# Performance work log

Hardware: AMD Instinct MI355X
Metric: run time of the kernel (lower is better)

Reference implementation:

```python
import jax, jax.numpy as jnp
import numpy as np

# ---- config (matches init_kwargs) ----
DIM = 1024
HEADS = 8            # local_heads == heads
QK_HD = 128          # qk_head_dim
V_HD = 128           # v_head_dim
NOPE = 64            # qk_nope_head_dim
ROPE = 64            # qk_rope_head_dim
KV_LORA = 256
N_EXP = 32
N_GROUPS = 8
TOPK = 4             # n_activated_experts
TOPK_GROUPS = 4
INTER = 512
N_SHARED = 1
ROUTE_SCALE = 1.0
EPS = 1e-6


def rmsnorm(x, w):
    xf = x.astype(jnp.float32)
    rms = jnp.sqrt(jnp.mean(xf ** 2, axis=-1, keepdims=True) + EPS)
    return (xf / rms * w).astype(x.dtype)


def setup_inputs() -> dict:
    key = jax.random.key(0)
    ks = jax.random.split(key, 16)
    s = 0.02
    return {
        "x": jax.random.normal(ks[0], (2, 1024, DIM), jnp.float32),
        # attention sub-layer params
        "norm_attn": jnp.ones((DIM,), jnp.float32),
        "wq": jax.random.normal(ks[1], (DIM, HEADS * QK_HD), jnp.float32) * s,
        "wkv_a": jax.random.normal(ks[2], (DIM, KV_LORA + ROPE), jnp.float32) * s,
        "kv_norm_w": jnp.ones((KV_LORA,), jnp.float32),
        "wkv_b": jax.random.normal(ks[3], (KV_LORA, HEADS * (NOPE + V_HD)), jnp.float32) * s,
        "wo": jax.random.normal(ks[4], (HEADS * V_HD, DIM), jnp.float32) * s,
        # MoE sub-layer params
        "norm_moe": jnp.ones((DIM,), jnp.float32),
        "gate_w": jax.random.normal(ks[5], (N_EXP, DIM), jnp.float32) * 0.01,
        "gate_b": jnp.zeros((N_EXP,), jnp.float32),
        "ew1": jax.random.normal(ks[6], (N_EXP, DIM, INTER), jnp.float32) * s,
        "ew2": jax.random.normal(ks[7], (N_EXP, INTER, DIM), jnp.float32) * s,
        "ew3": jax.random.normal(ks[8], (N_EXP, DIM, INTER), jnp.float32) * s,
        "sw1": jax.random.normal(ks[9], (DIM, N_SHARED * INTER), jnp.float32) * s,
        "sw2": jax.random.normal(ks[10], (N_SHARED * INTER, DIM), jnp.float32) * s,
        "sw3": jax.random.normal(ks[11], (DIM, N_SHARED * INTER), jnp.float32) * s,
    }


def _mla(x, wq, wkv_a, kv_norm_w, wkv_b, wo):
    B, S, _ = x.shape
    # q_lora_rank == 0 -> direct q projection; nope/rope split+concat is identity
    q = (x @ wq).reshape(B, S, HEADS, QK_HD)
    kv = x @ wkv_a                                   # [B,S,KV_LORA+ROPE]
    c, k_pe = kv[..., :KV_LORA], kv[..., KV_LORA:]
    kvp = (rmsnorm(c, kv_norm_w) @ wkv_b).reshape(B, S, HEADS, NOPE + V_HD)
    k_nope, v = kvp[..., :NOPE], kvp[..., NOPE:]
    k = jnp.concatenate(
        [k_nope, jnp.broadcast_to(k_pe[:, :, None, :], (B, S, HEADS, ROPE))], axis=-1)
    out = jax.nn.dot_product_attention(q, k, v, scale=QK_HD ** -0.5, is_causal=True)
    return out.reshape(B, S, -1) @ wo


def _gate(xf, gate_w, gate_b):
    T = xf.shape[0]
    scores = jax.nn.sigmoid(xf @ gate_w.T)           # [T,E]
    original = scores
    s = scores + gate_b
    # hierarchical group selection: top-2 score sum per group, keep top groups
    sg = s.reshape(T, N_GROUPS, -1)
    group_score = jnp.sort(sg, axis=-1)[..., -2:].sum(axis=-1)
    group_idx = jnp.argsort(group_score, axis=-1)[..., -TOPK_GROUPS:]
    mask = jnp.ones((T, N_GROUPS), bool).at[jnp.arange(T)[:, None], group_idx].set(False)
    s = jnp.where(mask[..., None], -jnp.inf, sg).reshape(T, -1)
    indices = jnp.argsort(s, axis=-1)[..., -TOPK:]   # [T,K]
    w = jnp.take_along_axis(original, indices, axis=1)
    w = w / (w.sum(axis=-1, keepdims=True) + 1e-20)  # sigmoid normalization
    return w * ROUTE_SCALE, indices


def _moe(xf, gate_w, gate_b, ew1, ew2, ew3, sw1, sw2, sw3):
    # dense all-expert SwiGLU as in the original (nn.vmap over axis_size=E)
    weights, indices = _gate(xf, gate_w, gate_b)
    h = jax.nn.silu(jnp.einsum('td,edh->eth', xf, ew1)) * jnp.einsum('td,edh->eth', xf, ew3)
    all_out = jnp.einsum('eth,ehd->etd', h, ew2)     # [E,T,dim]
    # per-token gather of its top-k experts, weighted combine
    selected = jnp.take_along_axis(all_out.transpose(1, 0, 2), indices[:, :, None], axis=1)  # [T,K,dim]
    y = (selected * weights[..., None]).sum(axis=1)
    z = (jax.nn.silu(xf @ sw1) * (xf @ sw3)) @ sw2   # shared expert MLP
    return y + z


def reference(x, norm_attn, wq, wkv_a, kv_norm_w, wkv_b, wo,
              norm_moe, gate_w, gate_b, ew1, ew2, ew3, sw1, sw2, sw3):
    # MLA layer: x + MLA(RMSNorm(x))
    x = x + _mla(rmsnorm(x, norm_attn), wq, wkv_a, kv_norm_w, wkv_b, wo)
    # MoE layer: x + MoE(RMSNorm(x))
    shape = x.shape
    xf = rmsnorm(x, norm_moe).reshape(-1, DIM)
    y = _moe(xf, gate_w, gate_b, ew1, ew2, ew3, sw1, sw2, sw3)
    return x + y.reshape(shape)
```

## Files before the change

kernel.cpp:

```cpp
#include <hip/hip_runtime.h>
#include <hip/hip_bf16.h>

#define T_TOK 2048
#define DIM 1024
#define HEADS 8
#define QK_HD 128
#define V_HD 128
#define NOPE 64
#define ROPE 64
#define KV_LORA 256
#define N_EXP 32
#define TOPK 4
#define INTER 512
#define S_LEN 1024
#define KVP_W (HEADS * (NOPE + V_HD))

typedef __attribute__((ext_vector_type(8))) _Float16 f16x8;
typedef __attribute__((ext_vector_type(4))) float f32x4;

__device__ inline unsigned short f2h(float f) {
  union { _Float16 h; unsigned short u; } c;
  c.h = (_Float16)f;
  return c.u;
}
__device__ inline float h2f(unsigned short u) {
  union { _Float16 h; unsigned short u; } c;
  c.u = u;
  return (float)c.h;
}

__device__ inline int swz(int row, int col) {
  return row * 64 + (col ^ (((row & 7) ^ ((row & 3) << 1)) << 3));
}

__launch_bounds__(256)
__global__ void tcvt_k(const float* __restrict__ src, unsigned short* __restrict__ dst,
                       int K, int N) {
  int e = blockIdx.z;
  src += (size_t)e * K * N;
  dst += (size_t)e * K * N;
  int n0 = blockIdx.x * 32, k0 = blockIdx.y * 32;
  __shared__ float ts[32][33];
  int tid = threadIdx.x;
  int r = tid >> 3, c4 = (tid & 7) * 4;
  float4 v = *(const float4*)(src + (size_t)(k0 + r) * N + n0 + c4);
  ts[r][c4] = v.x; ts[r][c4 + 1] = v.y; ts[r][c4 + 2] = v.z; ts[r][c4 + 3] = v.w;
  __syncthreads();
  ushort4 o;
  o.x = f2h(ts[c4][r]);
  o.y = f2h(ts[c4 + 1][r]);
  o.z = f2h(ts[c4 + 2][r]);
  o.w = f2h(ts[c4 + 3][r]);
  *(ushort4*)(dst + (size_t)(n0 + r) * K + k0 + c4) = o;
}

__launch_bounds__(64)
__global__ void zero_counters_k(int* __restrict__ counts, int* __restrict__ fill) {
  int i = threadIdx.x;
  if (i < N_EXP) { counts[i] = 0; fill[i] = 0; }
}

__launch_bounds__(256)
__global__ void rmsnorm_k(const float* __restrict__ x, int in_stride, int width,
                          const float* __restrict__ w, unsigned short* __restrict__ out,
                          float* __restrict__ out2, int out_stride) {
  int row = blockIdx.x;
  const float* xr = x + (size_t)row * in_stride;
  float ss = 0.f;
  for (int i = threadIdx.x; i < width; i += 256) { float v = xr[i]; ss += v * v; }
  #pragma unroll
  for (int off = 32; off; off >>= 1) ss += __shfl_down(ss, off, 64);
  __shared__ float red[4];
  if ((threadIdx.x & 63) == 0) red[threadIdx.x >> 6] = ss;
  __syncthreads();
  if (threadIdx.x == 0) {
    float tot = red[0] + red[1] + red[2] + red[3];
    red[0] = rsqrtf(tot / (float)width + 1e-6f);
  }
  __syncthreads();
  float scale = red[0];
  for (int i = threadIdx.x; i < width; i += 256) {
    float v = xr[i] * scale * w[i];
    out[(size_t)row * out_stride + i] = f2h(v);
    if (out2) out2[(size_t)row * out_stride + i] = v;
  }
}

template <int RES, int OUTH>
__launch_bounds__(256)
__global__ void gemm_bt_k(const unsigned short* __restrict__ A,
                          const unsigned short* __restrict__ B,
                          const float* __restrict__ R, void* __restrict__ Cout,
                          int N, int K) {
  const int n0 = blockIdx.x * 64;
  const int m0 = blockIdx.y * 64;
  __shared__ __align__(16) unsigned short As[64 * 64];
  __shared__ __align__(16) unsigned short Bs[64 * 64];
  const int tid = threadIdx.x;
  const int lane = tid & 63, wave = tid >> 6;
  const int quad = lane >> 4, lm = lane & 15;
  const int wm = (wave >> 1) * 32, wn = (wave & 1) * 32;
  f32x4 acc[2][2] = {};
  const int sr = tid >> 2, sc = tid & 3;
  const unsigned short* Ap = A + (size_t)(m0 + sr) * K;
  const unsigned short* Bp = B + (size_t)(n0 + sr) * K;
  f16x8 a0 = *(const f16x8*)(Ap + sc * 8);
  f16x8 a1 = *(const f16x8*)(Ap + sc * 8 + 32);
  f16x8 b0 = *(const f16x8*)(Bp + sc * 8);
  f16x8 b1 = *(const f16x8*)(Bp + sc * 8 + 32);
  for (int k0 = 0; k0 < K; k0 += 64) {
    __syncthreads();
    *(f16x8*)&As[swz(sr, sc * 8)] = a0;
    *(f16x8*)&As[swz(sr, sc * 8 + 32)] = a1;
    *(f16x8*)&Bs[swz(sr, sc * 8)] = b0;
    *(f16x8*)&Bs[swz(sr, sc * 8 + 32)] = b1;
    __syncthreads();
    const int kn = k0 + 64;
    if (kn < K) {
      a0 = *(const f16x8*)(Ap + kn + sc * 8);
      a1 = *(const f16x8*)(Ap + kn + sc * 8 + 32);
      b0 = *(const f16x8*)(Bp + kn + sc * 8);
      b1 = *(const f16x8*)(Bp + kn + sc * 8 + 32);
    }
    #pragma unroll
    for (int ks = 0; ks < 2; ks++) {
      f16x8 af0 = *(const f16x8*)&As[swz(wm + lm, ks * 32 + quad * 8)];
      f16x8 af1 = *(const f16x8*)&As[swz(wm + 16 + lm, ks * 32 + quad * 8)];
      f16x8 bf0 = *(const f16x8*)&Bs[swz(wn + lm, ks * 32 + quad * 8)];
      f16x8 bf1 = *(const f16x8*)&Bs[swz(wn + 16 + lm, ks * 32 + quad * 8)];
      acc[0][0] = __builtin_amdgcn_mfma_f32_16x16x32_f16(af0, bf0, acc[0][0], 0, 0, 0);
      acc[0][1] = __builtin_amdgcn_mfma_f32_16x16x32_f16(af0, bf1, acc[0][1], 0, 0, 0);
      acc[1][0] = __builtin_amdgcn_mfma_f32_16x16x32_f16(af1, bf0, acc[1][0], 0, 0, 0);
      acc[1][1] = __builtin_amdgcn_mfma_f32_16x16x32_f16(af1, bf1, acc[1][1], 0, 0, 0);
    }
  }
  #pragma unroll
  for (int i = 0; i < 2; i++)
    #pragma unroll
    for (int j = 0; j < 2; j++) {
      int row = m0 + wm + i * 16 + quad * 4;
      int col = n0 + wn + j * 16 + lm;
      #pragma unroll
      for (int r = 0; r < 4; r++) {
        float v = acc[i][j][r];
        if (RES) v += R[(size_t)(row + r) * N + col];
        if (OUTH) ((unsigned short*)Cout)[(size_t)(row + r) * N + col] = f2h(v);
        else ((float*)Cout)[(size_t)(row + r) * N + col] = v;
      }
    }
}

__launch_bounds__(256)
__global__ void moe_up_k(const unsigned short* __restrict__ xfb,
                         const unsigned short* __restrict__ w1t,
                         const unsigned short* __restrict__ w3t,
                         unsigned short* __restrict__ hout,
                         const int* __restrict__ perm, const int* __restrict__ offs,
                         int Mfull) {
  const int e = blockIdx.z;
  int base = 0, count = Mfull;
  if (offs) { base = offs[e]; count = offs[e + 1] - base; }
  const int m0 = blockIdx.y * 64;
  if (m0 >= count) return;
  const int n0 = blockIdx.x * 64;
  const unsigned short* W1 = w1t + (size_t)e * (INTER * DIM);
  const unsigned short* W3 = w3t + (size_t)e * (INTER * DIM);
  __shared__ __align__(16) unsigned short As[64 * 64];
  __shared__ __align__(16) unsigned short B1s[64 * 64];
  __shared__ __align__(16) unsigned short B2s[64 * 64];
  __shared__ int toks[64];
  const int tid = threadIdx.x;
  if (tid < 64) {
    int g = m0 + tid;
    toks[tid] = (g < count) ? (perm ? (perm[base + g] >> 2) : g) : -1;
  }
  __syncthreads();
  const int lane = tid & 63, wave = tid >> 6;
  const int quad = lane >> 4, lm = lane & 15;
  const int wm = (wave >> 1) * 32, wn = (wave & 1) * 32;
  f32x4 acc1[2][2] = {};
  f32x4 acc2[2][2] = {};
  const int sr = tid >> 2, sc = tid & 3;
  const int tok = toks[sr];
  const unsigned short* Ap = xfb + (size_t)(tok < 0 ? 0 : tok) * DIM;
  const bool av = (tok >= 0);
  const unsigned short* B1p = W1 + (size_t)(n0 + sr) * DIM;
  const unsigned short* B2p = W3 + (size_t)(n0 + sr) * DIM;
  f16x8 a0 = {0,0,0,0,0,0,0,0}, a1 = {0,0,0,0,0,0,0,0};
  if (av) {
    a0 = *(const f16x8*)(Ap + sc * 8);
    a1 = *(const f16x8*)(Ap + sc * 8 + 32);
  }
  f16x8 b10 = *(const f16x8*)(B1p + sc * 8);
  f16x8 b11 = *(const f16x8*)(B1p + sc * 8 + 32);
  f16x8 b20 = *(const f16x8*)(B2p + sc * 8);
  f16x8 b21 = *(const f16x8*)(B2p + sc * 8 + 32);
  for (int k0 = 0; k0 < DIM; k0 += 64) {
    __syncthreads();
    *(f16x8*)&As[swz(sr, sc * 8)] = a0;
    *(f16x8*)&As[swz(sr, sc * 8 + 32)] = a1;
    *(f16x8*)&B1s[swz(sr, sc * 8)] = b10;
    *(f16x8*)&B1s[swz(sr, sc * 8 + 32)] = b11;
    *(f16x8*)&B2s[swz(sr, sc * 8)] = b20;
    *(f16x8*)&B2s[swz(sr, sc * 8 + 32)] = b21;
    __syncthreads();
    const int kn = k0 + 64;
    if (kn < DIM) {
      if (av) {
        a0 = *(const f16x8*)(Ap + kn + sc * 8);
        a1 = *(const f16x8*)(Ap + kn + sc * 8 + 32);
      }
      b10 = *(const f16x8*)(B1p + kn + sc * 8);
      b11 = *(const f16x8*)(B1p + kn + sc * 8 + 32);
      b20 = *(const f16x8*)(B2p + kn + sc * 8);
      b21 = *(const f16x8*)(B2p + kn + sc * 8 + 32);
    }
    #pragma unroll
    for (int ks = 0; ks < 2; ks++) {
      f16x8 af0 = *(const f16x8*)&As[swz(wm + lm, ks * 32 + quad * 8)];
      f16x8 af1 = *(const f16x8*)&As[swz(wm + 16 + lm, ks * 32 + quad * 8)];
      f16x8 b1f0 = *(const f16x8*)&B1s[swz(wn + lm, ks * 32 + quad * 8)];
      f16x8 b1f1 = *(const f16x8*)&B1s[swz(wn + 16 + lm, ks * 32 + quad * 8)];
      f16x8 b2f0 = *(const f16x8*)&B2s[swz(wn + lm, ks * 32 + quad * 8)];
      f16x8 b2f1 = *(const f16x8*)&B2s[swz(wn + 16 + lm, ks * 32 + quad * 8)];
      acc1[0][0] = __builtin_amdgcn_mfma_f32_16x16x32_f16(af0, b1f0, acc1[0][0], 0, 0, 0);
      acc1[0][1] = __builtin_amdgcn_mfma_f32_16x16x32_f16(af0, b1f1, acc1[0][1], 0, 0, 0);
      acc1[1][0] = __builtin_amdgcn_mfma_f32_16x16x32_f16(af1, b1f0, acc1[1][0], 0, 0, 0);
      acc1[1][1] = __builtin_amdgcn_mfma_f32_16x16x32_f16(af1, b1f1, acc1[1][1], 0, 0, 0);
      acc2[0][0] = __builtin_amdgcn_mfma_f32_16x16x32_f16(af0, b2f0, acc2[0][0], 0, 0, 0);
      acc2[0][1] = __builtin_amdgcn_mfma_f32_16x16x32_f16(af0, b2f1, acc2[0][1], 0, 0, 0);
      acc2[1][0] = __builtin_amdgcn_mfma_f32_16x16x32_f16(af1, b2f0, acc2[1][0], 0, 0, 0);
      acc2[1][1] = __builtin_amdgcn_mfma_f32_16x16x32_f16(af1, b2f1, acc2[1][1], 0, 0, 0);
    }
  }
  #pragma unroll
  for (int i = 0; i < 2; i++)
    #pragma unroll
    for (int j = 0; j < 2; j++) {
      int col = n0 + wn + j * 16 + lm;
      #pragma unroll
      for (int r = 0; r < 4; r++) {
        int g = m0 + wm + i * 16 + quad * 4 + r;
        if (g < count) {
          float u = acc1[i][j][r];
          float vv = acc2[i][j][r];
          float h = (u / (1.f + __expf(-u))) * vv;
          hout[(size_t)(base + g) * INTER + col] = f2h(h);
        }
      }
    }
}

__launch_bounds__(256)
__global__ void moe_down_k(const unsigned short* __restrict__ hbuf,
                           const unsigned short* __restrict__ w2t,
                           unsigned short* __restrict__ dout,
                           const int* __restrict__ offs, int Mfull) {
  const int e = blockIdx.z;
  int base = 0, count = Mfull;
  if (offs) { base = offs[e]; count = offs[e + 1] - base; }
  const int m0 = blockIdx.y * 64;
  if (m0 >= count) return;
  const int n0 = blockIdx.x * 64;
  const unsigned short* W2 = w2t + (size_t)e * (DIM * INTER);
  __shared__ __align__(16) unsigned short As[64 * 64];
  __shared__ __align__(16) unsigned short Bs[64 * 64];
  const int tid = threadIdx.x;
  const int lane = tid & 63, wave = tid >> 6;
  const int quad = lane >> 4, lm = lane & 15;
  const int wm = (wave >> 1) * 32, wn = (wave & 1) * 32;
  f32x4 acc[2][2] = {};
  const int sr = tid >> 2, sc = tid & 3;
  const int g_s = m0 + sr;
  const bool av = (g_s < count);
  const unsigned short* Ap = hbuf + (size_t)(base + (av ? g_s : 0)) * INTER;
  const unsigned short* Bp = W2 + (size_t)(n0 + sr) * INTER;
  f16x8 a0 = {0,0,0,0,0,0,0,0}, a1 = {0,0,0,0,0,0,0,0};
  if (av) {
    a0 = *(const f16x8*)(Ap + sc * 8);
    a1 = *(const f16x8*)(Ap + sc * 8 + 32);
  }
  f16x8 b0 = *(const f16x8*)(Bp + sc * 8);
  f16x8 b1 = *(const f16x8*)(Bp + sc * 8 + 32);
  for (int k0 = 0; k0 < INTER; k0 += 64) {
    __syncthreads();
    *(f16x8*)&As[swz(sr, sc * 8)] = a0;
    *(f16x8*)&As[swz(sr, sc * 8 + 32)] = a1;
    *(f16x8*)&Bs[swz(sr, sc * 8)] = b0;
    *(f16x8*)&Bs[swz(sr, sc * 8 + 32)] = b1;
    __syncthreads();
    const int kn = k0 + 64;
    if (kn < INTER) {
      if (av) {
        a0 = *(const f16x8*)(Ap + kn + sc * 8);
        a1 = *(const f16x8*)(Ap + kn + sc * 8 + 32);
      }
      b0 = *(const f16x8*)(Bp + kn + sc * 8);
      b1 = *(const f16x8*)(Bp + kn + sc * 8 + 32);
    }
    #pragma unroll
    for (int ks = 0; ks < 2; ks++) {
      f16x8 af0 = *(const f16x8*)&As[swz(wm + lm, ks * 32 + quad * 8)];
      f16x8 af1 = *(const f16x8*)&As[swz(wm + 16 + lm, ks * 32 + quad * 8)];
      f16x8 bf0 = *(const f16x8*)&Bs[swz(wn + lm, ks * 32 + quad * 8)];
      f16x8 bf1 = *(const f16x8*)&Bs[swz(wn + 16 + lm, ks * 32 + quad * 8)];
      acc[0][0] = __builtin_amdgcn_mfma_f32_16x16x32_f16(af0, bf0, acc[0][0], 0, 0, 0);
      acc[0][1] = __builtin_amdgcn_mfma_f32_16x16x32_f16(af0, bf1, acc[0][1], 0, 0, 0);
      acc[1][0] = __builtin_amdgcn_mfma_f32_16x16x32_f16(af1, bf0, acc[1][0], 0, 0, 0);
      acc[1][1] = __builtin_amdgcn_mfma_f32_16x16x32_f16(af1, bf1, acc[1][1], 0, 0, 0);
    }
  }
  #pragma unroll
  for (int i = 0; i < 2; i++)
    #pragma unroll
    for (int j = 0; j < 2; j++) {
      int col = n0 + wn + j * 16 + lm;
      #pragma unroll
      for (int r = 0; r < 4; r++) {
        int g = m0 + wm + i * 16 + quad * 4 + r;
        if (g < count)
          dout[(size_t)(base + g) * DIM + col] = f2h(acc[i][j][r]);
      }
    }
}

__launch_bounds__(256)
__global__ void vtrans_k(const unsigned short* __restrict__ kvp,
                         unsigned short* __restrict__ vT) {
  const int z = blockIdx.z, h = z & 7, b = z >> 3;
  const int s0 = blockIdx.x * 32, d0 = blockIdx.y * 32;
  __shared__ unsigned short ts[32][36];
  const int tid = threadIdx.x;
  const int r = tid >> 3, c4 = (tid & 7) * 4;
  ushort4 v = *(const ushort4*)(kvp + (size_t)(b * S_LEN + s0 + r) * KVP_W + h * 192 + 64 + d0 + c4);
  ts[r][c4] = v.x; ts[r][c4 + 1] = v.y; ts[r][c4 + 2] = v.z; ts[r][c4 + 3] = v.w;
  __syncthreads();
  ushort4 o;
  o.x = ts[c4][r]; o.y = ts[c4 + 1][r]; o.z = ts[c4 + 2][r]; o.w = ts[c4 + 3][r];
  *(ushort4*)(vT + ((size_t)z * 128 + d0 + r) * S_LEN + s0 + c4) = o;
}

__launch_bounds__(256)
__global__ void attn_part_k(const unsigned short* __restrict__ q,
                            const unsigned short* __restrict__ kvp,
                            const float* __restrict__ kvb,
                            const unsigned short* __restrict__ vT,
                            float* __restrict__ opart, float* __restrict__ ml) {
  const int qt = blockIdx.x, ch = blockIdx.y, z = blockIdx.z;
  const int kt0 = ch * 4;
  if (kt0 > qt) return;
  const int h = z & 7, b = z >> 3;
  __shared__ __align__(16) _Float16 Ks[64][136];
  __shared__ __align__(16) _Float16 Vt[128][72];
  __shared__ __align__(16) _Float16 Ps[4][16][72];
  const int tid = threadIdx.x;
  const int lane = tid & 63, wave = tid >> 6;
  const int quad = lane >> 4, lm = lane & 15;
  const int qr0 = wave * 16;
  const float scale = 0.08838834764831845f;
  const int tq = b * S_LEN + qt * 64;

  f16x8 qf[4];
  #pragma unroll
  for (int kc = 0; kc < 4; kc++)
    qf[kc] = *(const f16x8*)(q + (size_t)(tq + qr0 + lm) * 1024 + h * 128 + kc * 32 + quad * 8);

  float m_i[4], l_i[4];
  #pragma unroll
  for (int r = 0; r < 4; r++) { m_i[r] = -1e30f; l_i[r] = 0.f; }
  f32x4 o_acc[8] = {};

  const int kt_end = (kt0 + 3 < qt) ? (kt0 + 3) : qt;
  for (int kt = kt0; kt <= kt_end; ++kt) {
    const int tk = b * S_LEN + kt * 64;
    for (int i = tid; i < 64 * 8; i += 256) {
      int key = i & 63, g = i >> 6;
      *(f16x8*)&Ks[key][g * 8] =
          *(const f16x8*)(kvp + (size_t)(tk + key) * KVP_W + h * 192 + g * 8);
    }
    for (int i = tid; i < 64 * 16; i += 256) {
      int key = i & 63, g = i >> 6;
      float4 v = *(const float4*)(kvb + (size_t)(tk + key) * 320 + 256 + g * 4);
      ushort4 u;
      u.x = f2h(v.x); u.y = f2h(v.y); u.z = f2h(v.z); u.w = f2h(v.w);
      *(ushort4*)&Ks[key][64 + g * 4] = u;
    }
    for (int i = tid; i < 128 * 8; i += 256) {
      int d = i >> 3, seg = i & 7;
      *(f16x8*)&Vt[d][seg * 8] =
          *(const f16x8*)(vT + ((size_t)z * 128 + d) * S_LEN + kt * 64 + seg * 8);
    }
    __syncthreads();

    f32x4 sacc[4] = {};
    #pragma unroll
    for (int kc = 0; kc < 4; kc++) {
      #pragma unroll
      for (int jn = 0; jn < 4; jn++) {
        f16x8 bf = *(const f16x8*)&Ks[jn * 16 + lm][kc * 32 + quad * 8];
        sacc[jn] = __builtin_amdgcn_mfma_f32_16x16x32_f16(qf[kc], bf, sacc[jn], 0, 0, 0);
      }
    }
    const bool diag = (kt == qt);
    float p[4][4];
    float rowmax[4], rowsum[4];
    #pragma unroll
    for (int r = 0; r < 4; r++) rowmax[r] = -1e30f;
    #pragma unroll
    for (int jn = 0; jn < 4; jn++)
      #pragma unroll
      for (int r = 0; r < 4; r++) {
        float s = sacc[jn][r] * scale;
        if (diag && (jn * 16 + lm > qr0 + quad * 4 + r)) s = -1e30f;
        p[jn][r] = s;
        rowmax[r] = fmaxf(rowmax[r], s);
      }
    #pragma unroll
    for (int m = 1; m < 16; m <<= 1)
      #pragma unroll
      for (int r = 0; r < 4; r++)
        rowmax[r] = fmaxf(rowmax[r], __shfl_xor(rowmax[r], m, 64));
    float al[4];
    #pragma unroll
    for (int r = 0; r < 4; r++) {
      float mn = fmaxf(m_i[r], rowmax[r]);
      al[r] = __expf(m_i[r] - mn);
      m_i[r] = mn;
      rowsum[r] = 0.f;
    }
    #pragma unroll
    for (int jn = 0; jn < 4; jn++)
      #pragma unroll
      for (int r = 0; r < 4; r++) {
        float pv = __expf(p[jn][r] - m_i[r]);
        p[jn][r] = pv;
        rowsum[r] += pv;
      }
    #pragma unroll
    for (int m = 1; m < 16; m <<= 1)
      #pragma unroll
      for (int r = 0; r < 4; r++)
        rowsum[r] += __shfl_xor(rowsum[r], m, 64);
    #pragma unroll
    for (int r = 0; r < 4; r++) l_i[r] = l_i[r] * al[r] + rowsum[r];
    #pragma unroll
    for (int jn2 = 0; jn2 < 8; jn2++)
      #pragma unroll
      for (int r = 0; r < 4; r++) o_acc[jn2][r] *= al[r];
    #pragma unroll
    for (int jn = 0; jn < 4; jn++)
      #pragma unroll
      for (int r = 0; r < 4; r++)
        Ps[wave][quad * 4 + r][jn * 16 + lm] = (_Float16)p[jn][r];
    #pragma unroll
    for (int kc = 0; kc < 2; kc++) {
      f16x8 af = *(const f16x8*)&Ps[wave][lm][kc * 32 + quad * 8];
      #pragma unroll
      for (int jn2 = 0; jn2 < 8; jn2++) {
        f16x8 bf = *(const f16x8*)&Vt[jn2 * 16 + lm][kc * 32 + quad * 8];
        o_acc[jn2] = __builtin_amdgcn_mfma_f32_16x16x32_f16(af, bf, o_acc[jn2], 0, 0, 0);
      }
    }
    __syncthreads();
  }

  const size_t slot = ((size_t)z * 16 + qt) * 4 + ch;
  float* op = opart + slot * 8192;
  #pragma unroll
  for (int jn2 = 0; jn2 < 8; jn2++) {
    int col = jn2 * 16 + lm;
    #pragma unroll
    for (int r = 0; r < 4; r++) {
      int row = qr0 + quad * 4 + r;
      op[(size_t)row * 128 + col] = o_acc[jn2][r];
    }
  }
  if (lm == 0) {
    #pragma unroll
    for (int r = 0; r < 4; r++) {
      int row = qr0 + quad * 4 + r;
      ml[slot * 128 + row * 2] = m_i[r];
      ml[slot * 128 + row * 2 + 1] = l_i[r];
    }
  }
}

__launch_bounds__(256)
__global__ void attn_comb_k(const float* __restrict__ opart, const float* __restrict__ ml,
                            unsigned short* __restrict__ o) {
  const int qt = blockIdx.x, z = blockIdx.y;
  const int h = z & 7, b = z >> 3;
  const int nch = (qt >> 2) + 1;
  const int tid = threadIdx.x;
  const int colg = tid & 31;
  const int tq = b * S_LEN + qt * 64;
  const size_t slotbase = ((size_t)z * 16 + qt) * 4;
  for (int row = tid >> 5; row < 64; row += 8) {
    float mmax = -1e30f;
    #pragma unroll
    for (int c = 0; c < 4; c++)
      if (c < nch) mmax = fmaxf(mmax, ml[(slotbase + c) * 128 + row * 2]);
    float w[4];
    float lsum = 0.f;
    #pragma unroll
    for (int c = 0; c < 4; c++) {
      if (c < nch) {
        float mc = ml[(slotbase + c) * 128 + row * 2];
        float lc = ml[(slotbase + c) * 128 + row * 2 + 1];
        w[c] = __expf(mc - mmax);
        lsum += lc * w[c];
      } else w[c] = 0.f;
    }
    float inv = 1.f / lsum;
    float ax = 0.f, ay = 0.f, az = 0.f, aw = 0.f;
    #pragma unroll
    for (int c = 0; c < 4; c++) {
      if (c < nch) {
        const float* op = opart + (slotbase + c) * 8192 + (size_t)row * 128 + colg * 4;
        float4 v = *(const float4*)op;
        ax += w[c] * v.x; ay += w[c] * v.y; az += w[c] * v.z; aw += w[c] * v.w;
      }
    }
    ushort4 u;
    u.x = f2h(ax * inv); u.y = f2h(ay * inv);
    u.z = f2h(az * inv); u.w = f2h(aw * inv);
    *(ushort4*)(o + (size_t)(tq + row) * 1024 + h * 128 + colg * 4) = u;
  }
}

__launch_bounds__(256)
__global__ void scores_k(const float* __restrict__ xf, const float* __restrict__ gw,
                         float* __restrict__ sc) {
  __shared__ float xls[32][129];
  __shared__ float gls[32][129];
  const int t0 = blockIdx.x * 32;
  const int tid = threadIdx.x;
  const int lr = tid >> 3, lc = tid & 7;
  const int e = tid & 31, tg = tid >> 5;
  float acc[4] = {};
  for (int k0 = 0; k0 < DIM; k0 += 128) {
    __syncthreads();
    #pragma unroll
    for (int it = 0; it < 4; it++) {
      int col = lc * 4 + it * 32;
      *(float4*)&xls[lr][col] = *(const float4*)(xf + (size_t)(t0 + lr) * DIM + k0 + col);
      *(float4*)&gls[lr][col] = *(const float4*)(gw + (size_t)lr * DIM + k0 + col);
    }
    __syncthreads();
    for (int d = 0; d < 128; d++) {
      float g = gls[e][d];
      #pragma unroll
      for (int j = 0; j < 4; j++)
        acc[j] += xls[tg * 4 + j][d] * g;
    }
  }
  #pragma unroll
  for (int j = 0; j < 4; j++)
    sc[(size_t)(t0 + tg * 4 + j) * N_EXP + e] = acc[j];
}

__launch_bounds__(64)
__global__ void route_k(const float* __restrict__ sc, const float* __restrict__ gb,
                        float* __restrict__ tw, int* __restrict__ tidx,
                        int* __restrict__ counts) {
  int t = blockIdx.x * 64 + threadIdx.x;
  if (t >= T_TOK) return;
  float orig[N_EXP], sb[N_EXP];
  #pragma unroll
  for (int i = 0; i < N_EXP; i++) {
    float s = 1.f / (1.f + __expf(-sc[(size_t)t * N_EXP + i]));
    orig[i] = s;
    sb[i] = s + gb[i];
  }
  float gsc[8];
  #pragma unroll
  for (int g = 0; g < 8; g++) {
    float m1 = -1e30f, m2 = -1e30f;
    #pragma unroll
    for (int j = 0; j < 4; j++) {
      float v = sb[g * 4 + j];
      if (v > m1) { m2 = m1; m1 = v; } else if (v > m2) m2 = v;
    }
    gsc[g] = m1 + m2;
  }
  unsigned gok = 0;
  #pragma unroll
  for (int it = 0; it < 4; it++) {
    int best = 0; float bv = -1e30f;
    #pragma unroll
    for (int g = 0; g < 8; g++)
      if (!((gok >> g) & 1u) && gsc[g] >= bv) { bv = gsc[g]; best = g; }
    gok |= 1u << best;
  }
  unsigned emask = 0;
  #pragma unroll
  for (int g = 0; g < 8; g++)
    if ((gok >> g) & 1u) emask |= 0xFu << (g * 4);
  unsigned taken = 0;
  int idx[TOPK]; float ow[TOPK]; float wsum = 0.f;
  #pragma unroll
  for (int k = 0; k < TOPK; k++) {
    int best = 0; float bv = -1e30f, bo = 0.f;
    #pragma unroll
    for (int i = 0; i < N_EXP; i++)
      if (((emask >> i) & 1u) && !((taken >> i) & 1u) && sb[i] >= bv) {
        bv = sb[i]; best = i; bo = orig[i];
      }
    taken |= 1u << best;
    idx[k] = best; ow[k] = bo; wsum += bo;
  }
  float inv = 1.f / (wsum + 1e-20f);
  #pragma unroll
  for (int k = 0; k < TOPK; k++) {
    tidx[t * TOPK + k] = idx[k];
    tw[t * TOPK + k] = ow[k] * inv;
    atomicAdd(&counts[idx[k]], 1);
  }
}

__global__ void scan_k(const int* __restrict__ counts, int* __restrict__ offs) {
  if (threadIdx.x == 0 && blockIdx.x == 0) {
    int acc = 0;
    for (int e = 0; e < N_EXP; e++) { offs[e] = acc; acc += counts[e]; }
    offs[N_EXP] = acc;
  }
}

__launch_bounds__(256)
__global__ void scatter_k(const int* __restrict__ tidx, const int* __restrict__ offs,
                          int* __restrict__ fill, int* __restrict__ perm,
                          int* __restrict__ posOf) {
  int t = blockIdx.x * 256 + threadIdx.x;
  if (t >= T_TOK) return;
  for (int j = 0; j < TOPK; j++) {
    int e = tidx[t * TOPK + j];
    int pos = atomicAdd(&fill[e], 1);
    int p = offs[e] + pos;
    perm[p] = t * TOPK + j;
    posOf[t * TOPK + j] = p;
  }
}

__launch_bounds__(256)
__global__ void final_gather_k(const float* __restrict__ x1,
                               const unsigned short* __restrict__ dbuf,
                               const unsigned short* __restrict__ sdbuf,
                               const int* __restrict__ posOf,
                               const float* __restrict__ tw,
                               float* __restrict__ out) {
  int t = blockIdx.x;
  int c0 = threadIdx.x * 4;
  int p0 = posOf[t * 4 + 0], p1 = posOf[t * 4 + 1];
  int p2 = posOf[t * 4 + 2], p3 = posOf[t * 4 + 3];
  float w0 = tw[t * 4 + 0], w1 = tw[t * 4 + 1];
  float w2 = tw[t * 4 + 2], w3 = tw[t * 4 + 3];
  size_t tb = (size_t)t * DIM;
  #pragma unroll
  for (int i = 0; i < 4; i++) {
    int c = c0 + i;
    float v = x1[tb + c] + h2f(sdbuf[tb + c])
            + w0 * h2f(dbuf[(size_t)p0 * DIM + c])
            + w1 * h2f(dbuf[(size_t)p1 * DIM + c])
            + w2 * h2f(dbuf[(size_t)p2 * DIM + c])
            + w3 * h2f(dbuf[(size_t)p3 * DIM + c]);
    out[tb + c] = v;
  }
}

extern "C" void kernel_launch(void* const* d_in, const int* in_sizes, int n_in,
                              void* d_out, int out_size, void* d_ws, size_t ws_size,
                              hipStream_t stream) {
  const float* x        = (const float*)d_in[0];
  const float* norm_attn= (const float*)d_in[1];
  const float* wq       = (const float*)d_in[2];
  const float* wkv_a    = (const float*)d_in[3];
  const float* kv_norm_w= (const float*)d_in[4];
  const float* wkv_b    = (const float*)d_in[5];
  const float* wo       = (const float*)d_in[6];
  const float* norm_moe = (const float*)d_in[7];
  const float* gate_w   = (const float*)d_in[8];
  const float* gate_b   = (const float*)d_in[9];
  const float* ew1      = (const float*)d_in[10];
  const float* ew2      = (const float*)d_in[11];
  const float* ew3      = (const float*)d_in[12];
  const float* sw1      = (const float*)d_in[13];
  const float* sw2      = (const float*)d_in[14];
  const float* sw3      = (const float*)d_in[15];
  float* out = (float*)d_out;

  char* wp = (char*)d_ws;
  auto alloc = [&](size_t bytes) -> char* {
    char* r = wp;
    wp += (bytes + 255) & ~(size_t)255;
    return r;
  };
  typedef unsigned short us;
  us* wqT   = (us*)alloc(1048576 * 2);
  us* wkvaT = (us*)alloc(327680 * 2);
  us* wkvbT = (us*)alloc(393216 * 2);
  us* woT   = (us*)alloc(1048576 * 2);
  us* ew1T  = (us*)alloc((size_t)16777216 * 2);
  us* ew3T  = (us*)alloc((size_t)16777216 * 2);
  us* ew2T  = (us*)alloc((size_t)16777216 * 2);
  us* sw1T  = (us*)alloc(524288 * 2);
  us* sw3T  = (us*)alloc(524288 * 2);
  us* sw2T  = (us*)alloc(524288 * 2);
  us* xb    = (us*)alloc(2097152 * 2);
  us* cn    = (us*)alloc(524288 * 2);
  us* atn   = (us*)alloc(2097152 * 2);
  us* dbuf  = (us*)alloc((size_t)8388608 * 2);
  us* qb    = (us*)alloc(2097152 * 4);
  float* kvb  = (float*)alloc(655360 * 4);
  us* kvp   = (us*)alloc(3145728 * 4);
  float* x1   = (float*)alloc(2097152 * 4);
  float* xf32 = (float*)alloc(2097152 * 4);
  float* scb  = (float*)alloc(65536 * 4);
  float* twb  = (float*)alloc(8192 * 4);
  int* tidx   = (int*)alloc(8192 * 4);
  int* perm   = (int*)alloc(8192 * 4);
  int* posOf  = (int*)alloc(8192 * 4);
  int* counts = (int*)alloc(64 * 4);
  int* offs   = (int*)alloc(64 * 4);
  int* fill   = (int*)alloc(64 * 4);
  us* vT     = (us*)alloc((size_t)2 * 8 * 128 * 1024 * 2);
  float* mlb = (float*)alloc((size_t)1024 * 128 * 4);
  us* sdbuf = qb;
  us* hbuf  = kvp;
  us* hs    = hbuf + (size_t)8192 * 512;
  float* opart = (float*)ew1T;

  tcvt_k<<<dim3(32, 32, 1), 256, 0, stream>>>(wq, wqT, 1024, 1024);
  tcvt_k<<<dim3(10, 32, 1), 256, 0, stream>>>(wkv_a, wkvaT, 1024, 320);
  tcvt_k<<<dim3(48, 8, 1), 256, 0, stream>>>(wkv_b, wkvbT, 256, 1536);
  tcvt_k<<<dim3(32, 32, 1), 256, 0, stream>>>(wo, woT, 1024, 1024);

  rmsnorm_k<<<T_TOK, 256, 0, stream>>>(x, DIM, DIM, norm_attn, xb, nullptr, DIM);
  gemm_bt_k<0, 1><<<dim3(16, 32), 256, 0, stream>>>(xb, wqT, nullptr, qb, 1024, 1024);
  gemm_bt_k<0, 0><<<dim3(5, 32), 256, 0, stream>>>(xb, wkvaT, nullptr, kvb, 320, 1024);
  rmsnorm_k<<<T_TOK, 256, 0, stream>>>(kvb, 320, KV_LORA, kv_norm_w, cn, nullptr, KV_LORA);
  gemm_bt_k<0, 1><<<dim3(24, 32), 256, 0, stream>>>(cn, wkvbT, nullptr, kvp, 1536, 256);
  vtrans_k<<<dim3(32, 4, 16), 256, 0, stream>>>(kvp, vT);
  attn_part_k<<<dim3(16, 4, 16), 256, 0, stream>>>(qb, kvp, kvb, vT, opart, mlb);
  attn_comb_k<<<dim3(16, 16), 256, 0, stream>>>(opart, mlb, atn);
  gemm_bt_k<1, 0><<<dim3(16, 32), 256, 0, stream>>>(atn, woT, x, x1, 1024, 1024);

  tcvt_k<<<dim3(16, 32, 32), 256, 0, stream>>>(ew1, ew1T, 1024, 512);
  tcvt_k<<<dim3(16, 32, 32), 256, 0, stream>>>(ew3, ew3T, 1024, 512);
  tcvt_k<<<dim3(32, 16, 32), 256, 0, stream>>>(ew2, ew2T, 512, 1024);
  tcvt_k<<<dim3(16, 32, 1), 256, 0, stream>>>(sw1, sw1T, 1024, 512);
  tcvt_k<<<dim3(16, 32, 1), 256, 0, stream>>>(sw3, sw3T, 1024, 512);
  tcvt_k<<<dim3(32, 16, 1), 256, 0, stream>>>(sw2, sw2T, 512, 1024);

  rmsnorm_k<<<T_TOK, 256, 0, stream>>>(x1, DIM, DIM, norm_moe, xb, xf32, DIM);
  zero_counters_k<<<1, 64, 0, stream>>>(counts, fill);
  scores_k<<<T_TOK / 32, 256, 0, stream>>>(xf32, gate_w, scb);
  route_k<<<T_TOK / 64, 64, 0, stream>>>(scb, gate_b, twb, tidx, counts);
  scan_k<<<1, 1, 0, stream>>>(counts, offs);
  scatter_k<<<(T_TOK + 255) / 256, 256, 0, stream>>>(tidx, offs, fill, perm, posOf);
  moe_up_k<<<dim3(8, 32, 32), 256, 0, stream>>>(xb, ew1T, ew3T, hbuf, perm, offs, 0);
  moe_down_k<<<dim3(16, 32, 32), 256, 0, stream>>>(hbuf, ew2T, dbuf, offs, 0);
  moe_up_k<<<dim3(8, 32, 1), 256, 0, stream>>>(xb, sw1T, sw3T, hs, nullptr, nullptr, T_TOK);
  moe_down_k<<<dim3(16, 32, 1), 256, 0, stream>>>(hs, sw2T, sdbuf, nullptr, T_TOK);

  final_gather_k<<<T_TOK, 256, 0, stream>>>(x1, dbuf, sdbuf, posOf, twb, out);
}
```

Baseline: 546.6 us.

## Fuse fp32-to-fp16 expert weight conversion into routed MoE GEMM kernels

Drops the separate transpose-and-convert passes over all 32 experts' w1/w3/w2 weights. New MoE up/down kernels read the fp32 weights directly, convert them to fp16 in registers and transpose them into shared memory. This removes a full extra read and write of about 200MB of expert weights. The cost is that each active tile reloads fp32 weights, doubling per-tile weight bytes, and uses a strided float4 load pattern. Shared-expert conversions are moved earlier but otherwise unchanged.

```diff
diff --git a/kernel.cpp b/kernel.cpp
--- a/kernel.cpp
+++ b/kernel.cpp
@@ -27,6 +27,9 @@
   union { _Float16 h; unsigned short u; } c;
   c.u = u;
   return (float)c.h;
+}
+__device__ inline float f4c(const float4& v, int c) {
+  return c == 0 ? v.x : c == 1 ? v.y : c == 2 ? v.z : v.w;
 }
 
 __device__ inline int swz(int row, int col) {
@@ -297,6 +300,197 @@
       }
       b0 = *(const f16x8*)(Bp + kn + sc * 8);
       b1 = *(const f16x8*)(Bp + kn + sc * 8 + 32);
+    }
+    #pragma unroll
+    for (int ks = 0; ks < 2; ks++) {
+      f16x8 af0 = *(const f16x8*)&As[swz(wm + lm, ks * 32 + quad * 8)];
+      f16x8 af1 = *(const f16x8*)&As[swz(wm + 16 + lm, ks * 32 + quad * 8)];
+      f16x8 bf0 = *(const f16x8*)&Bs[swz(wn + lm, ks * 32 + quad * 8)];
+      f16x8 bf1 = *(const f16x8*)&Bs[swz(wn + 16 + lm, ks * 32 + quad * 8)];
+      acc[0][0] = __builtin_amdgcn_mfma_f32_16x16x32_f16(af0, bf0, acc[0][0], 0, 0, 0);
+      acc[0][1] = __builtin_amdgcn_mfma_f32_16x16x32_f16(af0, bf1, acc[0][1], 0, 0, 0);
+      acc[1][0] = __builtin_amdgcn_mfma_f32_16x16x32_f16(af1, bf0, acc[1][0], 0, 0, 0);
+      acc[1][1] = __builtin_amdgcn_mfma_f32_16x16x32_f16(af1, bf1, acc[1][1], 0, 0, 0);
+    }
+  }
+  #pragma unroll
+  for (int i = 0; i < 2; i++)
+    #pragma unroll
+    for (int j = 0; j < 2; j++) {
+      int col = n0 + wn + j * 16 + lm;
+      #pragma unroll
+      for (int r = 0; r < 4; r++) {
+        int g = m0 + wm + i * 16 + quad * 4 + r;
+        if (g < count)
+          dout[(size_t)(base + g) * DIM + col] = f2h(acc[i][j][r]);
+      }
+    }
+}
+
+__launch_bounds__(256)
+__global__ void moe_up_f32_k(const unsigned short* __restrict__ xfb,
+                             const float* __restrict__ w1,
+                             const float* __restrict__ w3,
+                             unsigned short* __restrict__ hout,
+                             const int* __restrict__ perm,
+                             const int* __restrict__ offs) {
+  const int e = blockIdx.z;
+  const int base = offs[e];
+  const int count = offs[e + 1] - base;
+  const int m0 = blockIdx.y * 64;
+  if (m0 >= count) return;
+  const int n0 = blockIdx.x * 64;
+  const float* W1 = w1 + (size_t)e * (DIM * INTER);
+  const float* W3 = w3 + (size_t)e * (DIM * INTER);
+  __shared__ __align__(16) unsigned short As[64 * 64];
+  __shared__ __align__(16) unsigned short B1s[64 * 64];
+  __shared__ __align__(16) unsigned short B2s[64 * 64];
+  __shared__ int toks[64];
+  const int tid = threadIdx.x;
+  if (tid < 64) {
+    int g = m0 + tid;
+    toks[tid] = (g < count) ? (perm[base + g] >> 2) : -1;
+  }
+  __syncthreads();
+  const int lane = tid & 63, wave = tid >> 6;
+  const int quad = lane >> 4, lm = lane & 15;
+  const int wm = (wave >> 1) * 32, wn = (wave & 1) * 32;
+  f32x4 acc1[2][2] = {};
+  f32x4 acc2[2][2] = {};
+  const int sr = tid >> 2, sc = tid & 3;
+  const int tok = toks[sr];
+  const unsigned short* Ap = xfb + (size_t)(tok < 0 ? 0 : tok) * DIM;
+  const bool av = (tok >= 0);
+  const int ng = (tid & 15) * 4, kg = (tid >> 4) * 4;
+  const float* B1p = W1 + (size_t)kg * INTER + n0 + ng;
+  const float* B2p = W3 + (size_t)kg * INTER + n0 + ng;
+  f16x8 a0 = {0,0,0,0,0,0,0,0}, a1 = {0,0,0,0,0,0,0,0};
+  if (av) {
+    a0 = *(const f16x8*)(Ap + sc * 8);
+    a1 = *(const f16x8*)(Ap + sc * 8 + 32);
+  }
+  float4 b1v[4], b2v[4];
+  #pragma unroll
+  for (int j = 0; j < 4; j++) {
+    b1v[j] = *(const float4*)(B1p + (size_t)j * INTER);
+    b2v[j] = *(const float4*)(B2p + (size_t)j * INTER);
+  }
+  for (int k0 = 0; k0 < DIM; k0 += 64) {
+    __syncthreads();
+    *(f16x8*)&As[swz(sr, sc * 8)] = a0;
+    *(f16x8*)&As[swz(sr, sc * 8 + 32)] = a1;
+    #pragma unroll
+    for (int c = 0; c < 4; c++) {
+      ushort4 u1, u2;
+      u1.x = f2h(f4c(b1v[0], c)); u1.y = f2h(f4c(b1v[1], c));
+      u1.z = f2h(f4c(b1v[2], c)); u1.w = f2h(f4c(b1v[3], c));
+      u2.x = f2h(f4c(b2v[0], c)); u2.y = f2h(f4c(b2v[1], c));
+      u2.z = f2h(f4c(b2v[2], c)); u2.w = f2h(f4c(b2v[3], c));
+      *(ushort4*)&B1s[swz(ng + c, kg)] = u1;
+      *(ushort4*)&B2s[swz(ng + c, kg)] = u2;
+    }
+    __syncthreads();
+    const int kn = k0 + 64;
+    if (kn < DIM) {
+      if (av) {
+        a0 = *(const f16x8*)(Ap + kn + sc * 8);
+        a1 = *(const f16x8*)(Ap + kn + sc * 8 + 32);
+      }
+      #pragma unroll
+      for (int j = 0; j < 4; j++) {
+        b1v[j] = *(const float4*)(B1p + (size_t)(kn + j) * INTER);
+        b2v[j] = *(const float4*)(B2p + (size_t)(kn + j) * INTER);
+      }
+    }
+    #pragma unroll
+    for (int ks = 0; ks < 2; ks++) {
+      f16x8 af0 = *(const f16x8*)&As[swz(wm + lm, ks * 32 + quad * 8)];
+      f16x8 af1 = *(const f16x8*)&As[swz(wm + 16 + lm, ks * 32 + quad * 8)];
+      f16x8 b1f0 = *(const f16x8*)&B1s[swz(wn + lm, ks * 32 + quad * 8)];
+      f16x8 b1f1 = *(const f16x8*)&B1s[swz(wn + 16 + lm, ks * 32 + quad * 8)];
+      f16x8 b2f0 = *(const f16x8*)&B2s[swz(wn + lm, ks * 32 + quad * 8)];
+      f16x8 b2f1 = *(const f16x8*)&B2s[swz(wn + 16 + lm, ks * 32 + quad * 8)];
+      acc1[0][0] = __builtin_amdgcn_mfma_f32_16x16x32_f16(af0, b1f0, acc1[0][0], 0, 0, 0);
+      acc1[0][1] = __builtin_amdgcn_mfma_f32_16x16x32_f16(af0, b1f1, acc1[0][1], 0, 0, 0);
+      acc1[1][0] = __builtin_amdgcn_mfma_f32_16x16x32_f16(af1, b1f0, acc1[1][0], 0, 0, 0);
+      acc1[1][1] = __builtin_amdgcn_mfma_f32_16x16x32_f16(af1, b1f1, acc1[1][1], 0, 0, 0);
+      acc2[0][0] = __builtin_amdgcn_mfma_f32_16x16x32_f16(af0, b2f0, acc2[0][0], 0, 0, 0);
+      acc2[0][1] = __builtin_amdgcn_mfma_f32_16x16x32_f16(af0, b2f1, acc2[0][1], 0, 0, 0);
+      acc2[1][0] = __builtin_amdgcn_mfma_f32_16x16x32_f16(af1, b2f0, acc2[1][0], 0, 0, 0);
+      acc2[1][1] = __builtin_amdgcn_mfma_f32_16x16x32_f16(af1, b2f1, acc2[1][1], 0, 0, 0);
+    }
+  }
+  #pragma unroll
+  for (int i = 0; i < 2; i++)
+    #pragma unroll
+    for (int j = 0; j < 2; j++) {
+      int col = n0 + wn + j * 16 + lm;
+      #pragma unroll
+      for (int r = 0; r < 4; r++) {
+        int g = m0 + wm + i * 16 + quad * 4 + r;
+        if (g < count) {
+          float u = acc1[i][j][r];
+          float vv = acc2[i][j][r];
+          float h = (u / (1.f + __expf(-u))) * vv;
+          hout[(size_t)(base + g) * INTER + col] = f2h(h);
+        }
+      }
+    }
+}
+
+__launch_bounds__(256)
+__global__ void moe_down_f32_k(const unsigned short* __restrict__ hbuf,
+                               const float* __restrict__ w2,
+                               unsigned short* __restrict__ dout,
+                               const int* __restrict__ offs) {
+  const int e = blockIdx.z;
+  const int base = offs[e];
+  const int count = offs[e + 1] - base;
+  const int m0 = blockIdx.y * 64;
+  if (m0 >= count) return;
+  const int n0 = blockIdx.x * 64;
+  const float* W2 = w2 + (size_t)e * (INTER * DIM);
+  __shared__ __align__(16) unsigned short As[64 * 64];
+  __shared__ __align__(16) unsigned short Bs[64 * 64];
+  const int tid = threadIdx.x;
+  const int lane = tid & 63, wave = tid >> 6;
+  const int quad = lane >> 4, lm = lane & 15;
+  const int wm = (wave >> 1) * 32, wn = (wave & 1) * 32;
+  f32x4 acc[2][2] = {};
+  const int sr = tid >> 2, sc = tid & 3;
+  const int g_s = m0 + sr;
+  const bool av = (g_s < count);
+  const unsigned short* Ap = hbuf + (size_t)(base + (av ? g_s : 0)) * INTER;
+  const int ng = (tid & 15) * 4, kg = (tid >> 4) * 4;
+  const float* Bp = W2 + (size_t)kg * DIM + n0 + ng;
+  f16x8 a0 = {0,0,0,0,0,0,0,0}, a1 = {0,0,0,0,0,0,0,0};
+  if (av) {
+    a0 = *(const f16x8*)(Ap + sc * 8);
+    a1 = *(const f16x8*)(Ap + sc * 8 + 32);
+  }
+  float4 bv[4];
+  #pragma unroll
+  for (int j = 0; j < 4; j++) bv[j] = *(const float4*)(Bp + (size_t)j * DIM);
+  for (int k0 = 0; k0 < INTER; k0 += 64) {
+    __syncthreads();
+    *(f16x8*)&As[swz(sr, sc * 8)] = a0;
+    *(f16x8*)&As[swz(sr, sc * 8 + 32)] = a1;
+    #pragma unroll
+    for (int c = 0; c < 4; c++) {
+      ushort4 u;
+      u.x = f2h(f4c(bv[0], c)); u.y = f2h(f4c(bv[1], c));
+      u.z = f2h(f4c(bv[2], c)); u.w = f2h(f4c(bv[3], c));
+      *(ushort4*)&Bs[swz(ng + c, kg)] = u;
+    }
+    __syncthreads();
+    const int kn = k0 + 64;
+    if (kn < INTER) {
+      if (av) {
+        a0 = *(const f16x8*)(Ap + kn + sc * 8);
+        a1 = *(const f16x8*)(Ap + kn + sc * 8 + 32);
+      }
+      #pragma unroll
+      for (int j = 0; j < 4; j++) bv[j] = *(const float4*)(Bp + (size_t)(kn + j) * DIM);
     }
     #pragma unroll
     for (int ks = 0; ks < 2; ks++) {
@@ -733,6 +927,9 @@
   tcvt_k<<<dim3(10, 32, 1), 256, 0, stream>>>(wkv_a, wkvaT, 1024, 320);
   tcvt_k<<<dim3(48, 8, 1), 256, 0, stream>>>(wkv_b, wkvbT, 256, 1536);
   tcvt_k<<<dim3(32, 32, 1), 256, 0, stream>>>(wo, woT, 1024, 1024);
+  tcvt_k<<<dim3(16, 32, 1), 256, 0, stream>>>(sw1, sw1T, 1024, 512);
+  tcvt_k<<<dim3(16, 32, 1), 256, 0, stream>>>(sw3, sw3T, 1024, 512);
+  tcvt_k<<<dim3(32, 16, 1), 256, 0, stream>>>(sw2, sw2T, 512, 1024);
 
   rmsnorm_k<<<T_TOK, 256, 0, stream>>>(x, DIM, DIM, norm_attn, xb, nullptr, DIM);
   gemm_bt_k<0, 1><<<dim3(16, 32), 256, 0, stream>>>(xb, wqT, nullptr, qb, 1024, 1024);
@@ -744,21 +941,14 @@
   attn_comb_k<<<dim3(16, 16), 256, 0, stream>>>(opart, mlb, atn);
   gemm_bt_k<1, 0><<<dim3(16, 32), 256, 0, stream>>>(atn, woT, x, x1, 1024, 1024);
 
-  tcvt_k<<<dim3(16, 32, 32), 256, 0, stream>>>(ew1, ew1T, 1024, 512);
-  tcvt_k<<<dim3(16, 32, 32), 256, 0, stream>>>(ew3, ew3T, 1024, 512);
-  tcvt_k<<<dim3(32, 16, 32), 256, 0, stream>>>(ew2, ew2T, 512, 1024);
-  tcvt_k<<<dim3(16, 32, 1), 256, 0, stream>>>(sw1, sw1T, 1024, 512);
-  tcvt_k<<<dim3(16, 32, 1), 256, 0, stream>>>(sw3, sw3T, 1024, 512);
-  tcvt_k<<<dim3(32, 16, 1), 256, 0, stream>>>(sw2, sw2T, 512, 1024);
-
   rmsnorm_k<<<T_TOK, 256, 0, stream>>>(x1, DIM, DIM, norm_moe, xb, xf32, DIM);
   zero_counters_k<<<1, 64, 0, stream>>>(counts, fill);
   scores_k<<<T_TOK / 32, 256, 0, stream>>>(xf32, gate_w, scb);
   route_k<<<T_TOK / 64, 64, 0, stream>>>(scb, gate_b, twb, tidx, counts);
   scan_k<<<1, 1, 0, stream>>>(counts, offs);
   scatter_k<<<(T_TOK + 255) / 256, 256, 0, stream>>>(tidx, offs, fill, perm, posOf);
-  moe_up_k<<<dim3(8, 32, 32), 256, 0, stream>>>(xb, ew1T, ew3T, hbuf, perm, offs, 0);
-  moe_down_k<<<dim3(16, 32, 32), 256, 0, stream>>>(hbuf, ew2T, dbuf, offs, 0);
+  moe_up_f32_k<<<dim3(8, 32, 32), 256, 0, stream>>>(xb, ew1, ew3, hbuf, perm, offs);
+  moe_down_f32_k<<<dim3(16, 32, 32), 256, 0, stream>>>(hbuf, ew2, dbuf, offs);
   moe_up_k<<<dim3(8, 32, 1), 256, 0, stream>>>(xb, sw1T, sw3T, hs, nullptr, nullptr, T_TOK);
   moe_down_k<<<dim3(16, 32, 1), 256, 0, stream>>>(hs, sw2T, sdbuf, nullptr, T_TOK);
 
```

After: 531.6 us. 2.7% less time.

## Load GEMM tiles directly global-to-LDS with swizzled source addressing

Applied to the files above, without the earlier changes.

Replaces the register-staged prefetch in the dense, MoE gate/up and MoE down GEMMs with global_load_lds direct-to-LDS 16-byte loads. The swizzle is moved onto the global source column so the LDS layout stays the same. This removes the VGPR round trip and the LDS store instructions, but it also drops the software prefetch overlap, so each tile load now stalls at the barrier. Padding rows now load token or row 0 instead of zeros, which leaves garbage in rows that the epilogue is presumably masking.

```diff
diff --git a/kernel.cpp b/kernel.cpp
--- a/kernel.cpp
+++ b/kernel.cpp
@@ -29,8 +29,15 @@
   return (float)c.h;
 }
 
+__device__ inline int smask(int row) { return (row & 7) ^ ((row & 3) << 1); }
 __device__ inline int swz(int row, int col) {
-  return row * 64 + (col ^ (((row & 7) ^ ((row & 3) << 1)) << 3));
+  return row * 64 + (col ^ (smask(row) << 3));
+}
+
+__device__ inline void gl16(const void* g, void* l) {
+  __builtin_amdgcn_global_load_lds(
+      (const __attribute__((address_space(1))) void*)g,
+      (__attribute__((address_space(3))) void*)l, 16, 0, 0);
 }
 
 __launch_bounds__(256)
@@ -101,27 +108,24 @@
   const int quad = lane >> 4, lm = lane & 15;
   const int wm = (wave >> 1) * 32, wn = (wave & 1) * 32;
   f32x4 acc[2][2] = {};
-  const int sr = tid >> 2, sc = tid & 3;
-  const unsigned short* Ap = A + (size_t)(m0 + sr) * K;
-  const unsigned short* Bp = B + (size_t)(n0 + sr) * K;
-  f16x8 a0 = *(const f16x8*)(Ap + sc * 8);
-  f16x8 a1 = *(const f16x8*)(Ap + sc * 8 + 32);
-  f16x8 b0 = *(const f16x8*)(Bp + sc * 8);
-  f16x8 b1 = *(const f16x8*)(Bp + sc * 8 + 32);
+  const int r0 = wave * 16 + (lane >> 3), r1 = r0 + 8;
+  const int c0 = ((lane & 7) ^ smask(r0)) * 8;
+  const int c1 = ((lane & 7) ^ smask(r1)) * 8;
+  const unsigned short* A0 = A + (size_t)(m0 + r0) * K + c0;
+  const unsigned short* A1 = A + (size_t)(m0 + r1) * K + c1;
+  const unsigned short* B0 = B + (size_t)(n0 + r0) * K + c0;
+  const unsigned short* B1 = B + (size_t)(n0 + r1) * K + c1;
+  unsigned short* lA0 = &As[(size_t)(wave * 16) * 64];
+  unsigned short* lA1 = &As[(size_t)(wave * 16 + 8) * 64];
+  unsigned short* lB0 = &Bs[(size_t)(wave * 16) * 64];
+  unsigned short* lB1 = &Bs[(size_t)(wave * 16 + 8) * 64];
   for (int k0 = 0; k0 < K; k0 += 64) {
     __syncthreads();
-    *(f16x8*)&As[swz(sr, sc * 8)] = a0;
-    *(f16x8*)&As[swz(sr, sc * 8 + 32)] = a1;
-    *(f16x8*)&Bs[swz(sr, sc * 8)] = b0;
-    *(f16x8*)&Bs[swz(sr, sc * 8 + 32)] = b1;
-    __syncthreads();
-    const int kn = k0 + 64;
-    if (kn < K) {
-      a0 = *(const f16x8*)(Ap + kn + sc * 8);
-      a1 = *(const f16x8*)(Ap + kn + sc * 8 + 32);
-      b0 = *(const f16x8*)(Bp + kn + sc * 8);
-      b1 = *(const f16x8*)(Bp + kn + sc * 8 + 32);
-    }
+    gl16(A0 + k0, lA0);
+    gl16(A1 + k0, lA1);
+    gl16(B0 + k0, lB0);
+    gl16(B1 + k0, lB1);
+    __syncthreads();
     #pragma unroll
     for (int ks = 0; ks < 2; ks++) {
       f16x8 af0 = *(const f16x8*)&As[swz(wm + lm, ks * 32 + quad * 8)];
@@ -180,41 +184,32 @@
   const int wm = (wave >> 1) * 32, wn = (wave & 1) * 32;
   f32x4 acc1[2][2] = {};
   f32x4 acc2[2][2] = {};
-  const int sr = tid >> 2, sc = tid & 3;
-  const int tok = toks[sr];
-  const unsigned short* Ap = xfb + (size_t)(tok < 0 ? 0 : tok) * DIM;
-  const bool av = (tok >= 0);
-  const unsigned short* B1p = W1 + (size_t)(n0 + sr) * DIM;
-  const unsigned short* B2p = W3 + (size_t)(n0 + sr) * DIM;
-  f16x8 a0 = {0,0,0,0,0,0,0,0}, a1 = {0,0,0,0,0,0,0,0};
-  if (av) {
-    a0 = *(const f16x8*)(Ap + sc * 8);
-    a1 = *(const f16x8*)(Ap + sc * 8 + 32);
-  }
-  f16x8 b10 = *(const f16x8*)(B1p + sc * 8);
-  f16x8 b11 = *(const f16x8*)(B1p + sc * 8 + 32);
-  f16x8 b20 = *(const f16x8*)(B2p + sc * 8);
-  f16x8 b21 = *(const f16x8*)(B2p + sc * 8 + 32);
+  const int r0 = wave * 16 + (lane >> 3), r1 = r0 + 8;
+  const int c0 = ((lane & 7) ^ smask(r0)) * 8;
+  const int c1 = ((lane & 7) ^ smask(r1)) * 8;
+  int tk0 = toks[r0]; if (tk0 < 0) tk0 = 0;
+  int tk1 = toks[r1]; if (tk1 < 0) tk1 = 0;
+  const unsigned short* A0 = xfb + (size_t)tk0 * DIM + c0;
+  const unsigned short* A1 = xfb + (size_t)tk1 * DIM + c1;
+  const unsigned short* B10 = W1 + (size_t)(n0 + r0) * DIM + c0;
+  const unsigned short* B11 = W1 + (size_t)(n0 + r1) * DIM + c1;
+  const unsigned short* B20 = W3 + (size_t)(n0 + r0) * DIM + c0;
+  const unsigned short* B21 = W3 + (size_t)(n0 + r1) * DIM + c1;
+  unsigned short* lA0 = &As[(size_t)(wave * 16) * 64];
+  unsigned short* lA1 = &As[(size_t)(wave * 16 + 8) * 64];
+  unsigned short* lB10 = &B1s[(size_t)(wave * 16) * 64];
+  unsigned short* lB11 = &B1s[(size_t)(wave * 16 + 8) * 64];
+  unsigned short* lB20 = &B2s[(size_t)(wave * 16) * 64];
+  unsigned short* lB21 = &B2s[(size_t)(wave * 16 + 8) * 64];
   for (int k0 = 0; k0 < DIM; k0 += 64) {
     __syncthreads();
-    *(f16x8*)&As[swz(sr, sc * 8)] = a0;
-    *(f16x8*)&As[swz(sr, sc * 8 + 32)] = a1;
-    *(f16x8*)&B1s[swz(sr, sc * 8)] = b10;
-    *(f16x8*)&B1s[swz(sr, sc * 8 + 32)] = b11;
-    *(f16x8*)&B2s[swz(sr, sc * 8)] = b20;
-    *(f16x8*)&B2s[swz(sr, sc * 8 + 32)] = b21;
-    __syncthreads();
-    const int kn = k0 + 64;
-    if (kn < DIM) {
-      if (av) {
-        a0 = *(const f16x8*)(Ap + kn + sc * 8);
-        a1 = *(const f16x8*)(Ap + kn + sc * 8 + 32);
-      }
-      b10 = *(const f16x8*)(B1p + kn + sc * 8);
-      b11 = *(const f16x8*)(B1p + kn + sc * 8 + 32);
-      b20 = *(const f16x8*)(B2p + kn + sc * 8);
-      b21 = *(const f16x8*)(B2p + kn + sc * 8 + 32);
-    }
+    gl16(A0 + k0, lA0);
+    gl16(A1 + k0, lA1);
+    gl16(B10 + k0, lB10);
+    gl16(B11 + k0, lB11);
+    gl16(B20 + k0, lB20);
+    gl16(B21 + k0, lB21);
+    __syncthreads();
     #pragma unroll
     for (int ks = 0; ks < 2; ks++) {
       f16x8 af0 = *(const f16x8*)&As[swz(wm + lm, ks * 32 + quad * 8)];
@@ -270,34 +265,26 @@
   const int quad = lane >> 4, lm = lane & 15;
   const int wm = (wave >> 1) * 32, wn = (wave & 1) * 32;
   f32x4 acc[2][2] = {};
-  const int sr = tid >> 2, sc = tid & 3;
-  const int g_s = m0 + sr;
-  const bool av = (g_s < count);
-  const unsigned short* Ap = hbuf + (size_t)(base + (av ? g_s : 0)) * INTER;
-  const unsigned short* Bp = W2 + (size_t)(n0 + sr) * INTER;
-  f16x8 a0 = {0,0,0,0,0,0,0,0}, a1 = {0,0,0,0,0,0,0,0};
-  if (av) {
-    a0 = *(const f16x8*)(Ap + sc * 8);
-    a1 = *(const f16x8*)(Ap + sc * 8 + 32);
-  }
-  f16x8 b0 = *(const f16x8*)(Bp + sc * 8);
-  f16x8 b1 = *(const f16x8*)(Bp + sc * 8 + 32);
+  const int r0 = wave * 16 + (lane >> 3), r1 = r0 + 8;
+  const int c0 = ((lane & 7) ^ smask(r0)) * 8;
+  const int c1 = ((lane & 7) ^ smask(r1)) * 8;
+  int g0 = m0 + r0; if (g0 >= count) g0 = 0;
+  int g1 = m0 + r1; if (g1 >= count) g1 = 0;
+  const unsigned short* A0 = hbuf + (size_t)(base + g0) * INTER + c0;
+  const unsigned short* A1 = hbuf + (size_t)(base + g1) * INTER + c1;
+  const unsigned short* B0 = W2 + (size_t)(n0 + r0) * INTER + c0;
+  const unsigned short* B1 = W2 + (size_t)(n0 + r1) * INTER + c1;
+  unsigned short* lA0 = &As[(size_t)(wave * 16) * 64];
+  unsigned short* lA1 = &As[(size_t)(wave * 16 + 8) * 64];
+  unsigned short* lB0 = &Bs[(size_t)(wave * 16) * 64];
+  unsigned short* lB1 = &Bs[(size_t)(wave * 16 + 8) * 64];
   for (int k0 = 0; k0 < INTER; k0 += 64) {
     __syncthreads();
-    *(f16x8*)&As[swz(sr, sc * 8)] = a0;
-    *(f16x8*)&As[swz(sr, sc * 8 + 32)] = a1;
-    *(f16x8*)&Bs[swz(sr, sc * 8)] = b0;
-    *(f16x8*)&Bs[swz(sr, sc * 8 + 32)] = b1;
-    __syncthreads();
-    const int kn = k0 + 64;
-    if (kn < INTER) {
-      if (av) {
-        a0 = *(const f16x8*)(Ap + kn + sc * 8);
-        a1 = *(const f16x8*)(Ap + kn + sc * 8 + 32);
-      }
-      b0 = *(const f16x8*)(Bp + kn + sc * 8);
-      b1 = *(const f16x8*)(Bp + kn + sc * 8 + 32);
-    }
+    gl16(A0 + k0, lA0);
+    gl16(A1 + k0, lA1);
+    gl16(B0 + k0, lB0);
+    gl16(B1 + k0, lB1);
+    __syncthreads();
     #pragma unroll
     for (int ks = 0; ks < 2; ks++) {
       f16x8 af0 = *(const f16x8*)&As[swz(wm + lm, ks * 32 + quad * 8)];
```

After: 550.9 us. No clear change (+0.8%).
